# Kernel optimization log

Hardware: AMD Instinct MI355X
Metric: run time of the kernel (lower is better)

The kernel has to match this reference:

```python
import jax, jax.numpy as jnp
import numpy as np

N = 100000   # nodes
E = 1600000  # edges
IN, HID, OUT = 128, 128, 64  # hidden = 2 * out_channels per GCNEncoder


def setup_inputs() -> dict:
    key = jax.random.key(0)
    k = jax.random.split(key, 5)
    x = jax.random.normal(k[0], (N, IN), dtype=jnp.float32)
    edge_index = jax.random.randint(k[1], (2, E), 0, N, dtype=jnp.int32)
    # Glorot-style init like PyG GCNConv
    W1 = jax.random.normal(k[2], (IN, HID), dtype=jnp.float32) * (1.0 / np.sqrt(IN))
    b1 = jnp.zeros((HID,), dtype=jnp.float32)
    W2 = jax.random.normal(k[3], (HID, OUT), dtype=jnp.float32) * (1.0 / np.sqrt(HID))
    b2 = jnp.zeros((OUT,), dtype=jnp.float32)
    return {"x": x, "edge_index": edge_index, "W1": W1, "b1": b1, "W2": W2, "b2": b2}


def gcn_conv(x, row, col, W, b):
    # x: [N, F_in]; row/col: [E+N] (edge_index with self-loops appended)
    h = x @ W                                      # dense transform [N, F_out]
    deg = jax.ops.segment_sum(jnp.ones_like(col, dtype=h.dtype), col, num_segments=N)
    dinv = jnp.where(deg > 0, jax.lax.rsqrt(deg), 0.0)
    norm = dinv[row] * dinv[col]                   # symmetric normalization per edge
    msg = h[row] * norm[:, None]                   # gather + scale: [E+N, F_out]
    out = jax.ops.segment_sum(msg, col, num_segments=N)  # scatter-add to targets
    return out + b


def reference(x, edge_index, W1, b1, W2, b2):
    loops = jnp.arange(N, dtype=edge_index.dtype)
    row = jnp.concatenate([edge_index[0], loops])  # sources
    col = jnp.concatenate([edge_index[1], loops])  # targets
    h = jax.nn.relu(gcn_conv(x, row, col, W1, b1))
    return gcn_conv(h, row, col, W2, b2)
```

## Files before the change

kernel.cpp:

```cpp
#include <hip/hip_runtime.h>
#include <hip/hip_fp16.h>

#define N_NODES 100000
#define N_EDGES 1600000
#define K_DIM   128

#define CHUNK_LG 8
#define CHUNK    256
#define NBKT     ((N_NODES + CHUNK - 1) / CHUNK)
#define CAP      4608
#define EPB      4096
#define NBLK_A   ((N_EDGES + EPB - 1) / EPB)
#define G1_BLOCKS ((N_NODES + 63) / 64)
#define NBLK_TOT (G1_BLOCKS + NBLK_A)

typedef _Float16 half8 __attribute__((ext_vector_type(8)));
typedef float    f32x4 __attribute__((ext_vector_type(4)));

__global__ __launch_bounds__(256) void k_prepW(const float* __restrict__ W1,
                                               const float* __restrict__ W2,
                                               _Float16* __restrict__ Wt1,
                                               _Float16* __restrict__ Wt2) {
    int c = blockIdx.x * 256 + threadIdx.x;
    const float* W; _Float16* Wt; int nout;
    if (c < 2048) { W = W1; Wt = Wt1; nout = 128; }
    else          { W = W2; Wt = Wt2; nout = 64; c -= 2048; }
    int n  = c >> 4;
    int k0 = (c & 15) * 8;
    half8 v;
#pragma unroll
    for (int j = 0; j < 8; ++j)
        v[j] = (_Float16)W[(size_t)(k0 + j) * nout + n];
    *reinterpret_cast<half8*>(Wt + (size_t)n * K_DIM + k0) = v;
}

__global__ __launch_bounds__(256) void k_gemm1_bucket(
    const float* __restrict__ x, const _Float16* __restrict__ Wt,
    _Float16* __restrict__ Hout,
    const int* __restrict__ row, const int* __restrict__ col,
    int* __restrict__ gcur, int* __restrict__ pairs)
{
    __shared__ __align__(16) char smem[128 * 136 * 2];

    if (blockIdx.x % 5 != 0) {
        constexpr int KD = K_DIM, NOUT = 128, NT = NOUT / 16;
        _Float16 (*Blds)[KD + 8] = reinterpret_cast<_Float16(*)[KD + 8]>(smem);

        for (int i = threadIdx.x; i < NOUT * (KD / 8); i += 256) {
            int n = i >> 4, k0 = (i & 15) * 8;
            *reinterpret_cast<half8*>(&Blds[n][k0]) =
                *reinterpret_cast<const half8*>(Wt + (size_t)n * KD + k0);
        }
        __syncthreads();

        const int tile = blockIdx.x - blockIdx.x / 5 - 1;
        const int wave = threadIdx.x >> 6;
        const int lane = threadIdx.x & 63;
        const int r16  = lane & 15;
        const int kg   = lane >> 4;
        const int arow = tile * 64 + wave * 16 + r16;
        const bool rowok = arow < N_NODES;

        f32x4 acc[NT];
#pragma unroll
        for (int ct = 0; ct < NT; ++ct) acc[ct] = (f32x4){0.f, 0.f, 0.f, 0.f};

#pragma unroll
        for (int kc = 0; kc < KD / 32; ++kc) {
            const int k0 = kc * 32 + kg * 8;
            float4 xa = make_float4(0.f, 0.f, 0.f, 0.f), xb = xa;
            if (rowok) {
                const float4* ap = reinterpret_cast<const float4*>(
                    x + (size_t)arow * KD + k0);
                xa = ap[0]; xb = ap[1];
            }
            half8 a;
            a[0] = (_Float16)xa.x; a[1] = (_Float16)xa.y;
            a[2] = (_Float16)xa.z; a[3] = (_Float16)xa.w;
            a[4] = (_Float16)xb.x; a[5] = (_Float16)xb.y;
            a[6] = (_Float16)xb.z; a[7] = (_Float16)xb.w;
#pragma unroll
            for (int ct = 0; ct < NT; ++ct) {
                half8 b = *reinterpret_cast<const half8*>(&Blds[ct * 16 + r16][k0]);
                acc[ct] = __builtin_amdgcn_mfma_f32_16x16x32_f16(a, b, acc[ct], 0, 0, 0);
            }
        }

        const int orow0 = tile * 64 + wave * 16 + kg * 4;
#pragma unroll
        for (int r = 0; r < 4; ++r) {
            int orow = orow0 + r;
            if (orow < N_NODES) {
#pragma unroll
                for (int ct = 0; ct < NT; ++ct)
                    Hout[(size_t)orow * NOUT + ct * 16 + r16] = (_Float16)acc[ct][r];
            }
        }
    } else {
        int* hist  = (int*)smem;
        int* sbase = hist + 512;
        int* lcur  = hist + 1024;
        int t = threadIdx.x;
        for (int i = t; i < NBKT; i += 256) { hist[i] = 0; lcur[i] = 0; }
        __syncthreads();
        int base = (blockIdx.x / 5) * EPB;
        int myb[16], myp[16];
#pragma unroll
        for (int j = 0; j < 16; ++j) {
            int i = base + t + j * 256;
            int b = -1, p = 0;
            if (i < N_EDGES) {
                int r = row[i], c = col[i];
                b = c >> CHUNK_LG;
                p = ((c & (CHUNK - 1)) << 17) | r;
                atomicAdd(&hist[b], 1);
            }
            myb[j] = b; myp[j] = p;
        }
        __syncthreads();
        for (int i = t; i < NBKT; i += 256) {
            int c = hist[i];
            sbase[i] = c ? atomicAdd(&gcur[i], c) : 0;
        }
        __syncthreads();
#pragma unroll
        for (int j = 0; j < 16; ++j) {
            int b = myb[j];
            if (b >= 0) {
                int pos = sbase[b] + atomicAdd(&lcur[b], 1);
                pairs[b * CAP + pos] = myp[j];
            }
        }
    }
}

__global__ __launch_bounds__(256) void k_fillB(const int* __restrict__ gcur,
                                               const int* __restrict__ pairs,
                                               int* __restrict__ rowptr,
                                               float* __restrict__ dinv,
                                               int* __restrict__ srows) {
    __shared__ int mpl[CAP];
    __shared__ int red[256];
    __shared__ int psum[256];
    __shared__ int deg[CHUNK];
    __shared__ int curs[CHUNK];
    int b = blockIdx.x, t = threadIdx.x;

    int part = 0;
    for (int i = t; i < NBKT; i += 256)
        if (i < b) part += gcur[i];
    red[t] = part;
    deg[t] = 0;
    __syncthreads();
    for (int off = 128; off; off >>= 1) {
        if (t < off) red[t] += red[t + off];
        __syncthreads();
    }
    int gb = red[0];
    int cnt = gcur[b];
    if (b == 0 && t == 0) rowptr[N_NODES] = N_EDGES;

    int nbase = b << CHUNK_LG;
    const int* mp = pairs + b * CAP;

    for (int i = t; i < cnt; i += 256) {
        int v = mp[i];
        mpl[i] = v;
        atomicAdd(&deg[v >> 17], 1);
    }
    __syncthreads();

    int d = deg[t];
    psum[t] = d;
    __syncthreads();
    for (int off = 1; off < 256; off <<= 1) {
        int u = (t >= off) ? psum[t - off] : 0;
        __syncthreads();
        psum[t] += u;
        __syncthreads();
    }
    int o = gb + psum[t] - d;
    curs[t] = o;
    int node = nbase + t;
    if (node < N_NODES) {
        rowptr[node] = o;
        dinv[node] = rsqrtf(1.f + (float)d);
    }
    __syncthreads();
    for (int i = t; i < cnt; i += 256) {
        int v = mpl[i];
        int pos = atomicAdd(&curs[v >> 17], 1);
        srows[pos] = v & 0x1FFFF;
    }
}

template<int NOUT>
__global__ __launch_bounds__(256) void k_gemm_mfma2(
    const _Float16* __restrict__ Ah, const _Float16* __restrict__ Wt,
    const float* __restrict__ b_in, _Float16* __restrict__ Hout, int nrows)
{
    constexpr int KD = K_DIM;
    constexpr int NT = NOUT / 16;
    __shared__ _Float16 Blds[NOUT][KD + 8];

    for (int i = threadIdx.x; i < NOUT * (KD / 8); i += 256) {
        int n = i >> 4, k0 = (i & 15) * 8;
        *reinterpret_cast<half8*>(&Blds[n][k0]) =
            *reinterpret_cast<const half8*>(Wt + (size_t)n * KD + k0);
    }
    __syncthreads();

    const int wave = threadIdx.x >> 6;
    const int lane = threadIdx.x & 63;
    const int r16  = lane & 15;
    const int kg   = lane >> 4;
    const int arow = blockIdx.x * 64 + wave * 16 + r16;
    const bool rowok = arow < nrows;

    f32x4 acc[NT];
#pragma unroll
    for (int ct = 0; ct < NT; ++ct) acc[ct] = (f32x4){0.f, 0.f, 0.f, 0.f};

#pragma unroll
    for (int kc = 0; kc < KD / 32; ++kc) {
        const int k0 = kc * 32 + kg * 8;
        uint4 raw = make_uint4(0, 0, 0, 0);
        if (rowok)
            raw = *reinterpret_cast<const uint4*>(Ah + (size_t)arow * KD + k0);
        union { uint4 u; _Float16 h[8]; } U; U.u = raw;
        float4 bA = *reinterpret_cast<const float4*>(b_in + k0);
        float4 bB = *reinterpret_cast<const float4*>(b_in + k0 + 4);
        half8 a;
        a[0] = (_Float16)fmaxf((float)U.h[0] + bA.x, 0.f);
        a[1] = (_Float16)fmaxf((float)U.h[1] + bA.y, 0.f);
        a[2] = (_Float16)fmaxf((float)U.h[2] + bA.z, 0.f);
        a[3] = (_Float16)fmaxf((float)U.h[3] + bA.w, 0.f);
        a[4] = (_Float16)fmaxf((float)U.h[4] + bB.x, 0.f);
        a[5] = (_Float16)fmaxf((float)U.h[5] + bB.y, 0.f);
        a[6] = (_Float16)fmaxf((float)U.h[6] + bB.z, 0.f);
        a[7] = (_Float16)fmaxf((float)U.h[7] + bB.w, 0.f);
#pragma unroll
        for (int ct = 0; ct < NT; ++ct) {
            half8 b = *reinterpret_cast<const half8*>(&Blds[ct * 16 + r16][k0]);
            acc[ct] = __builtin_amdgcn_mfma_f32_16x16x32_f16(a, b, acc[ct], 0, 0, 0);
        }
    }

    const int orow0 = blockIdx.x * 64 + wave * 16 + kg * 4;
#pragma unroll
    for (int r = 0; r < 4; ++r) {
        int orow = orow0 + r;
        if (orow < nrows) {
#pragma unroll
            for (int ct = 0; ct < NT; ++ct)
                Hout[(size_t)orow * NOUT + ct * 16 + r16] = (_Float16)acc[ct][r];
        }
    }
}

__device__ __forceinline__ void fma8(uint4 v, float wgt, float (&acc)[8]) {
    union { uint4 u; _Float16 h[8]; } U;
    U.u = v;
#pragma unroll
    for (int j = 0; j < 8; ++j)
        acc[j] = fmaf((float)U.h[j], wgt, acc[j]);
}

template<int F, bool OUT_HALF>
__global__ __launch_bounds__(256) void k_gather_h(
    const int* __restrict__ rowptr, const int* __restrict__ srows,
    const float* __restrict__ dinv, const _Float16* __restrict__ H,
    const float* __restrict__ bias, void* __restrict__ OUT, int n)
{
    constexpr int LPR = F / 8;
    constexpr int GR  = 64 / LPR;
    int w = blockIdx.x * 4 + (threadIdx.x >> 6);
    if (w >= n) return;
    int lane = threadIdx.x & 63;
    int g = lane / LPR;
    int c = lane % LPR;
    float di = dinv[w];
    int s = rowptr[w], e = rowptr[w + 1];
    const uint4* Hp = reinterpret_cast<const uint4*>(H);

    float acc[8];
#pragma unroll
    for (int j = 0; j < 8; ++j) acc[j] = 0.f;
    uint4 hv = Hp[(size_t)w * LPR + c];
    fma8(hv, (g == 0) ? di * di : 0.f, acc);

    if (s < e) {
        int k0 = s + g;
        int kc = min(k0, e - 1);
        int r  = srows[kc];
        float wcur = (k0 < e) ? dinv[r] * di : 0.f;
        uint4 hcur = Hp[(size_t)r * LPR + c];
        for (int k = s + GR; k < e; k += GR) {
            int k1  = k + g;
            int kc1 = min(k1, e - 1);
            int r1  = srows[kc1];
            float wnxt = (k1 < e) ? dinv[r1] * di : 0.f;
            uint4 hnxt = Hp[(size_t)r1 * LPR + c];
            fma8(hcur, wcur, acc);
            wcur = wnxt; hcur = hnxt;
        }
        fma8(hcur, wcur, acc);
    }

#pragma unroll
    for (int m = 32; m >= LPR; m >>= 1) {
#pragma unroll
        for (int j = 0; j < 8; ++j)
            acc[j] += __shfl_xor(acc[j], m, 64);
    }

    if (g == 0) {
        if constexpr (OUT_HALF) {
            union { uint4 u; __half2 h[4]; } P;
#pragma unroll
            for (int j = 0; j < 4; ++j)
                P.h[j] = __floats2half2_rn(acc[2 * j], acc[2 * j + 1]);
            reinterpret_cast<uint4*>(OUT)[(size_t)w * LPR + c] = P.u;
        } else {
            const float4* bp = reinterpret_cast<const float4*>(bias + c * 8);
            float4 b0 = bp[0], b1v = bp[1];
            float4 o0 = make_float4(acc[0] + b0.x, acc[1] + b0.y,
                                    acc[2] + b0.z, acc[3] + b0.w);
            float4 o1 = make_float4(acc[4] + b1v.x, acc[5] + b1v.y,
                                    acc[6] + b1v.z, acc[7] + b1v.w);
            float* op = (float*)OUT + (size_t)w * F + c * 8;
            *reinterpret_cast<float4*>(op)     = o0;
            *reinterpret_cast<float4*>(op + 4) = o1;
        }
    }
}


extern "C" void kernel_launch(void* const* d_in, const int* in_sizes, int n_in,
                              void* d_out, int out_size, void* d_ws, size_t ws_size,
                              hipStream_t stream) {
    const float* x  = (const float*)d_in[0];
    const int*   ei = (const int*)  d_in[1];
    const float* W1 = (const float*)d_in[2];
    const float* b1 = (const float*)d_in[3];
    const float* W2 = (const float*)d_in[4];
    const float* b2 = (const float*)d_in[5];
    float* out = (float*)d_out;

    const int* row = ei;
    const int* col = ei + N_EDGES;

    char* ws = (char*)d_ws;
    int*   gcur   = (int*)ws;
    int*   rowptr = gcur + 512;
    float* dinv   = (float*)(rowptr + ((N_NODES + 256) & ~255));
    int*   srows  = (int*)(dinv + ((N_NODES + 255) & ~255));
    _Float16* bufH  = (_Float16*)(srows + ((N_EDGES + 255) & ~255));
    _Float16* bufAgg = bufH + (size_t)N_NODES * 128;
    _Float16* bufH2  = bufAgg + (size_t)N_NODES * 128;
    _Float16* Wt1 = bufH2 + (size_t)N_NODES * 64;
    _Float16* Wt2 = Wt1 + 128 * 128;
    int*   pairs  = (int*)(Wt2 + 64 * 128 + 256);

    hipMemsetAsync(gcur, 0, NBKT * sizeof(int), stream);
    k_prepW<<<12, 256, 0, stream>>>(W1, W2, Wt1, Wt2);

    k_gemm1_bucket<<<NBLK_TOT, 256, 0, stream>>>(
        x, Wt1, bufH, row, col, gcur, pairs);

    k_fillB<<<NBKT, 256, 0, stream>>>(gcur, pairs, rowptr, dinv, srows);

    k_gather_h<128, true><<<(N_NODES + 3) / 4, 256, 0, stream>>>(
        rowptr, srows, dinv, bufH, nullptr, bufAgg, N_NODES);

    k_gemm_mfma2<64><<<(N_NODES + 63) / 64, 256, 0, stream>>>(
        bufAgg, Wt2, b1, bufH2, N_NODES);

    k_gather_h<64, false><<<(N_NODES + 3) / 4, 256, 0, stream>>>(
        rowptr, srows, dinv, bufH2, b2, out, N_NODES);
}
```

Before: 191.8 us.

## Process two nodes per wave in gather and halve bucket chunk size

The neighbor-gather kernels now assign a half-wave to each destination node, so a wave handles two nodes and reduces over 32 lanes instead of 64. The CSR-building buckets shrink from 256 to 128 nodes, with a smaller per-bucket capacity, which doubles the bucket count and the shared histogram footprint. The separate memset of the bucket counters is folded into the weight-prep kernel as extra blocks, removing one launch. The trade-off is fewer rows in flight per node in the gather loop, and more buckets to prefix-sum in the fill kernel.

New measurement: 176.8 us, median of 2. -7.8%, faster.

```diff
diff --git a/kernel.cpp b/kernel.cpp
--- a/kernel.cpp
+++ b/kernel.cpp
@@ -5,10 +5,10 @@
 #define N_EDGES 1600000
 #define K_DIM   128
 
-#define CHUNK_LG 8
-#define CHUNK    256
+#define CHUNK_LG 7
+#define CHUNK    128
 #define NBKT     ((N_NODES + CHUNK - 1) / CHUNK)
-#define CAP      4608
+#define CAP      2560
 #define EPB      4096
 #define NBLK_A   ((N_EDGES + EPB - 1) / EPB)
 #define G1_BLOCKS ((N_NODES + 63) / 64)
@@ -20,7 +20,13 @@
 __global__ __launch_bounds__(256) void k_prepW(const float* __restrict__ W1,
                                                const float* __restrict__ W2,
                                                _Float16* __restrict__ Wt1,
-                                               _Float16* __restrict__ Wt2) {
+                                               _Float16* __restrict__ Wt2,
+                                               int* __restrict__ gcur) {
+    if (blockIdx.x >= 12) {
+        int i = (blockIdx.x - 12) * 256 + threadIdx.x;
+        if (i < NBKT) gcur[i] = 0;
+        return;
+    }
     int c = blockIdx.x * 256 + threadIdx.x;
     const float* W; _Float16* Wt; int nout;
     if (c < 2048) { W = W1; Wt = Wt1; nout = 128; }
@@ -98,8 +104,8 @@
         }
     } else {
         int* hist  = (int*)smem;
-        int* sbase = hist + 512;
-        int* lcur  = hist + 1024;
+        int* sbase = hist + 1024;
+        int* lcur  = hist + 2048;
         int t = threadIdx.x;
         for (int i = t; i < NBKT; i += 256) { hist[i] = 0; lcur[i] = 0; }
         __syncthreads();
@@ -128,7 +134,7 @@
             int b = myb[j];
             if (b >= 0) {
                 int pos = sbase[b] + atomicAdd(&lcur[b], 1);
-                pairs[b * CAP + pos] = myp[j];
+                pairs[(size_t)b * CAP + pos] = myp[j];
             }
         }
     }
@@ -141,7 +147,7 @@
                                                int* __restrict__ srows) {
     __shared__ int mpl[CAP];
     __shared__ int red[256];
-    __shared__ int psum[256];
+    __shared__ int psum[CHUNK];
     __shared__ int deg[CHUNK];
     __shared__ int curs[CHUNK];
     int b = blockIdx.x, t = threadIdx.x;
@@ -150,7 +156,7 @@
     for (int i = t; i < NBKT; i += 256)
         if (i < b) part += gcur[i];
     red[t] = part;
-    deg[t] = 0;
+    if (t < CHUNK) deg[t] = 0;
     __syncthreads();
     for (int off = 128; off; off >>= 1) {
         if (t < off) red[t] += red[t + off];
@@ -160,8 +166,7 @@
     int cnt = gcur[b];
     if (b == 0 && t == 0) rowptr[N_NODES] = N_EDGES;
 
-    int nbase = b << CHUNK_LG;
-    const int* mp = pairs + b * CAP;
+    const int* mp = pairs + (size_t)b * CAP;
 
     for (int i = t; i < cnt; i += 256) {
         int v = mp[i];
@@ -170,21 +175,23 @@
     }
     __syncthreads();
 
-    int d = deg[t];
-    psum[t] = d;
-    __syncthreads();
-    for (int off = 1; off < 256; off <<= 1) {
-        int u = (t >= off) ? psum[t - off] : 0;
-        __syncthreads();
-        psum[t] += u;
-        __syncthreads();
-    }
-    int o = gb + psum[t] - d;
-    curs[t] = o;
-    int node = nbase + t;
-    if (node < N_NODES) {
-        rowptr[node] = o;
-        dinv[node] = rsqrtf(1.f + (float)d);
+    int d = (t < CHUNK) ? deg[t] : 0;
+    if (t < CHUNK) psum[t] = d;
+    __syncthreads();
+    for (int off = 1; off < CHUNK; off <<= 1) {
+        int u = (t >= off && t < CHUNK) ? psum[t - off] : 0;
+        __syncthreads();
+        if (t < CHUNK) psum[t] += u;
+        __syncthreads();
+    }
+    if (t < CHUNK) {
+        int o = gb + psum[t] - d;
+        curs[t] = o;
+        int node = (b << CHUNK_LG) + t;
+        if (node < N_NODES) {
+            rowptr[node] = o;
+            dinv[node] = rsqrtf(1.f + (float)d);
+        }
     }
     __syncthreads();
     for (int i = t; i < cnt; i += 256) {
@@ -273,12 +280,14 @@
     const float* __restrict__ bias, void* __restrict__ OUT, int n)
 {
     constexpr int LPR = F / 8;
-    constexpr int GR  = 64 / LPR;
-    int w = blockIdx.x * 4 + (threadIdx.x >> 6);
+    constexpr int GR  = 32 / LPR;
+    int lane = threadIdx.x & 63;
+    int half = lane >> 5;
+    int hl   = lane & 31;
+    int w = blockIdx.x * 8 + (threadIdx.x >> 6) * 2 + half;
     if (w >= n) return;
-    int lane = threadIdx.x & 63;
-    int g = lane / LPR;
-    int c = lane % LPR;
+    int g = hl / LPR;
+    int c = hl % LPR;
     float di = dinv[w];
     int s = rowptr[w], e = rowptr[w + 1];
     const uint4* Hp = reinterpret_cast<const uint4*>(H);
@@ -308,7 +317,7 @@
     }
 
 #pragma unroll
-    for (int m = 32; m >= LPR; m >>= 1) {
+    for (int m = 16; m >= LPR; m >>= 1) {
 #pragma unroll
         for (int j = 0; j < 8; ++j)
             acc[j] += __shfl_xor(acc[j], m, 64);
@@ -352,7 +361,7 @@
 
     char* ws = (char*)d_ws;
     int*   gcur   = (int*)ws;
-    int*   rowptr = gcur + 512;
+    int*   rowptr = gcur + 1024;
     float* dinv   = (float*)(rowptr + ((N_NODES + 256) & ~255));
     int*   srows  = (int*)(dinv + ((N_NODES + 255) & ~255));
     _Float16* bufH  = (_Float16*)(srows + ((N_EDGES + 255) & ~255));
@@ -362,20 +371,19 @@
     _Float16* Wt2 = Wt1 + 128 * 128;
     int*   pairs  = (int*)(Wt2 + 64 * 128 + 256);
 
-    hipMemsetAsync(gcur, 0, NBKT * sizeof(int), stream);
-    k_prepW<<<12, 256, 0, stream>>>(W1, W2, Wt1, Wt2);
+    k_prepW<<<16, 256, 0, stream>>>(W1, W2, Wt1, Wt2, gcur);
 
     k_gemm1_bucket<<<NBLK_TOT, 256, 0, stream>>>(
         x, Wt1, bufH, row, col, gcur, pairs);
 
     k_fillB<<<NBKT, 256, 0, stream>>>(gcur, pairs, rowptr, dinv, srows);
 
-    k_gather_h<128, true><<<(N_NODES + 3) / 4, 256, 0, stream>>>(
+    k_gather_h<128, true><<<(N_NODES + 7) / 8, 256, 0, stream>>>(
         rowptr, srows, dinv, bufH, nullptr, bufAgg, N_NODES);
 
     k_gemm_mfma2<64><<<(N_NODES + 63) / 64, 256, 0, stream>>>(
         bufAgg, Wt2, b1, bufH2, N_NODES);
 
-    k_gather_h<64, false><<<(N_NODES + 3) / 4, 256, 0, stream>>>(
+    k_gather_h<64, false><<<(N_NODES + 7) / 8, 256, 0, stream>>>(
         rowptr, srows, dinv, bufH2, b2, out, N_NODES);
 }
```
